# Kernel optimization log

Measured on AMD Instinct MI355X. Metric: run time of the kernel, lower is better.

The kernel has to match this reference:

```python
import jax, jax.numpy as jnp
import numpy as np

G = 7          # 7x7 feature map -> 49 nodes per image
N = G * G
K = 3          # knn_k
NEG_SLOPE = 0.2  # PyG GATConv default leaky_relu slope


def build_spatial_edges():
    # 8-neighborhood grid edges on the 7x7 map, directed (src -> dst)
    src, dst = [], []
    for r in range(G):
        for c in range(G):
            i = r * G + c
            for dr in (-1, 0, 1):
                for dc in (-1, 0, 1):
                    if dr == 0 and dc == 0:
                        continue
                    rr, cc = r + dr, c + dc
                    if 0 <= rr < G and 0 <= cc < G:
                        src.append(rr * G + cc)
                        dst.append(i)
    return np.array([src, dst], dtype=np.int32)

SPATIAL = build_spatial_edges()  # [2, 312]


def build_edges(x):
    """x: [B, N, F] node features -> (src, dst) each [B, E].
    Edges = spatial 8-neighborhood + feature-space kNN (k=3) + self-loops."""
    B = x.shape[0]
    sq = jnp.sum(x * x, axis=-1)                               # [B, N]
    d = sq[:, :, None] + sq[:, None, :] - 2.0 * jnp.einsum('bnf,bmf->bnm', x, x)
    d = d + jnp.eye(N, dtype=x.dtype) * 1e9                    # exclude self
    _, nbr = jax.lax.top_k(-d, K)                              # [B, N, K]
    knn_src = nbr.reshape(B, N * K)
    knn_dst = jnp.broadcast_to(jnp.repeat(jnp.arange(N, dtype=jnp.int32), K)[None], (B, N * K))
    sp = jnp.asarray(SPATIAL)
    Es = sp.shape[1]
    loops = jnp.arange(N, dtype=jnp.int32)
    src = jnp.concatenate([jnp.broadcast_to(sp[0][None], (B, Es)), knn_src.astype(jnp.int32),
                           jnp.broadcast_to(loops[None], (B, N))], axis=1)
    dst = jnp.concatenate([jnp.broadcast_to(sp[1][None], (B, Es)), knn_dst,
                           jnp.broadcast_to(loops[None], (B, N))], axis=1)
    return src, dst


def gat_layer(x, src, dst, W, a_src, a_dst, b, concat):
    """PyG-style GATConv (eval mode, no dropout). x: [N,F], src/dst: [E]."""
    H, C = a_src.shape
    h = (x @ W).reshape(N, H, C)                               # [N, H, C]
    es = jnp.sum(h * a_src[None], axis=-1)                     # [N, H]
    ed = jnp.sum(h * a_dst[None], axis=-1)                     # [N, H]
    e = jax.nn.leaky_relu(es[src] + ed[dst], NEG_SLOPE)        # [E, H]
    m = jax.ops.segment_max(e, dst, num_segments=N)            # [N, H]
    m = jnp.where(jnp.isfinite(m), m, 0.0)
    p = jnp.exp(e - m[dst])
    denom = jax.ops.segment_sum(p, dst, num_segments=N)
    alpha = p / jnp.maximum(denom[dst], 1e-16)                 # softmax over incoming edges
    out = jax.ops.segment_sum(alpha[:, :, None] * h[src], dst, num_segments=N)  # [N, H, C]
    out = out.reshape(N, H * C) if concat else out.mean(axis=1)
    return out + b


def setup_inputs() -> dict:
    key = jax.random.key(0)
    ks = jax.random.split(key, 14)
    B, F, Hd, Cd, O, NC = 256, 1024, 8, 128, 256, 14
    s = 0.05
    return {
        'feat_map': jax.random.normal(ks[0], (B, F, G, G), dtype=jnp.float32),
        'W1': jax.random.normal(ks[1], (F, Hd * Cd), dtype=jnp.float32) * s,
        'a_src1': jax.random.normal(ks[2], (Hd, Cd), dtype=jnp.float32) * s,
        'a_dst1': jax.random.normal(ks[3], (Hd, Cd), dtype=jnp.float32) * s,
        'b1': jnp.zeros((Hd * Cd,), dtype=jnp.float32),
        'W2': jax.random.normal(ks[4], (Hd * Cd, O), dtype=jnp.float32) * s,
        'a_src2': jax.random.normal(ks[5], (1, O), dtype=jnp.float32) * s,
        'a_dst2': jax.random.normal(ks[6], (1, O), dtype=jnp.float32) * s,
        'b2': jnp.zeros((O,), dtype=jnp.float32),
        'Wc1': jax.random.normal(ks[7], (O, O), dtype=jnp.float32) * s,
        'bc1': jnp.zeros((O,), dtype=jnp.float32),
        'Wc2': jax.random.normal(ks[8], (O, NC), dtype=jnp.float32) * s,
        'bc2': jnp.zeros((NC,), dtype=jnp.float32),
    }


def reference(feat_map, W1, a_src1, a_dst1, b1, W2, a_src2, a_dst2, b2, Wc1, bc1, Wc2, bc2):
    B = feat_map.shape[0]
    # backbone output relu + flatten 7x7 map into 49 nodes
    x = jax.nn.relu(feat_map).reshape(B, -1, N).transpose(0, 2, 1)  # [B, N, 1024]
    src, dst = build_edges(x)

    def per_graph(xg, sg, dg):
        h = jax.nn.elu(gat_layer(xg, sg, dg, W1, a_src1, a_dst1, b1, True))
        h = jax.nn.elu(gat_layer(h, sg, dg, W2, a_src2, a_dst2, b2, False))
        return h.mean(axis=0)                                   # global mean pool -> [256]

    pooled = jax.vmap(per_graph)(x, src, dst)                   # [B, 256]
    return jax.nn.relu(pooled @ Wc1 + bc1) @ Wc2 + bc2          # [B, 14]
```

## Files before the change

kernel.cpp:

```cpp
#include <hip/hip_runtime.h>

#define GDIM 7
#define NN 49
#define FDIM 1024
#define HD 8
#define CD 128
#define ODIM 256
#define NC 14
#define MAXE 12

typedef __attribute__((ext_vector_type(4))) float f32x4;
typedef __attribute__((ext_vector_type(8))) short s16x8;

struct us4 { unsigned short x, y, z, w; };

__device__ __forceinline__ unsigned short f2bf(float x) {
  unsigned u = __float_as_uint(x);
  return (unsigned short)((u + 0x7fffu + ((u >> 16) & 1u)) >> 16);
}
__device__ __forceinline__ float bf2f(unsigned short h) {
  return __uint_as_float((unsigned)h << 16);
}

#define GLOAD_LDS16(g, l)                                          \
  __builtin_amdgcn_global_load_lds(                                \
      (const __attribute__((address_space(1))) void*)(g),          \
      (__attribute__((address_space(3))) void*)(l), 16, 0, 0)

__global__ void __launch_bounds__(256) relu_transpose_kernel(
    const float* __restrict__ F, float* __restrict__ X,
    unsigned short* __restrict__ Xh, unsigned short* __restrict__ Xl) {
  const int b  = blockIdx.x >> 4;
  const int f0 = (blockIdx.x & 15) << 6;
  const int tid = threadIdx.x;
  __shared__ float lds[64 * NN];
  const float* src = F + (size_t)b * FDIM * NN + (size_t)f0 * NN;
  for (int idx = tid; idx < 64 * NN; idx += 256) lds[idx] = src[idx];
  __syncthreads();
  for (int pass = 0; pass < 13; pass++) {
    int n = pass * 4 + (tid >> 6);
    int fi = tid & 63;
    if (n < NN) {
      float v = lds[fi * NN + n];
      v = v > 0.f ? v : 0.f;
      size_t o = ((size_t)b * NN + n) * FDIM + f0 + fi;
      X[o] = v;
      unsigned short h = f2bf(v);
      Xh[o] = h;
      Xl[o] = f2bf(v - bf2f(h));
    }
  }
}

__global__ void __launch_bounds__(256) knn_kernel(
    const float* __restrict__ X, int* __restrict__ srcs_g,
    int* __restrict__ cnt_g) {
  const int b = blockIdx.x, tid = threadIdx.x;
  __shared__ float xs[56][68];
  __shared__ float gram[56][57];
  const float* Xb = X + (size_t)b * NN * FDIM;

  const int tr = tid / 14, tc = tid % 14;
  float acc[4][4];
#pragma unroll
  for (int i = 0; i < 4; i++)
#pragma unroll
    for (int j = 0; j < 4; j++) acc[i][j] = 0.f;

  for (int c0 = 0; c0 < FDIM; c0 += 64) {
    __syncthreads();
    for (int idx = tid; idx < NN * 16; idx += 256) {
      int n = idx >> 4, q = idx & 15;
      *(float4*)&xs[n][q << 2] =
          *(const float4*)&Xb[(size_t)n * FDIM + c0 + (q << 2)];
    }
    __syncthreads();
    if (tid < 196) {
#pragma unroll
      for (int k4 = 0; k4 < 64; k4 += 4) {
        float4 a[4], bb[4];
#pragma unroll
        for (int i = 0; i < 4; i++) a[i]  = *(const float4*)&xs[tr + 14 * i][k4];
#pragma unroll
        for (int j = 0; j < 4; j++) bb[j] = *(const float4*)&xs[tc + 14 * j][k4];
#pragma unroll
        for (int i = 0; i < 4; i++)
#pragma unroll
          for (int j = 0; j < 4; j++)
            acc[i][j] += a[i].x * bb[j].x + a[i].y * bb[j].y +
                         a[i].z * bb[j].z + a[i].w * bb[j].w;
      }
    }
  }
  if (tid < 196) {
#pragma unroll
    for (int i = 0; i < 4; i++)
#pragma unroll
      for (int j = 0; j < 4; j++) gram[tr + 14 * i][tc + 14 * j] = acc[i][j];
  }
  __syncthreads();
  if (tid < NN) {
    const int n = tid;
    const float sqn = gram[n][n];
    float d0 = 1e30f, d1 = 1e30f, d2 = 1e30f;
    int i0 = 0, i1 = 0, i2 = 0;
    for (int m = 0; m < NN; m++) {
      if (m == n) continue;
      float d = sqn + gram[m][m] - 2.f * gram[n][m];
      if (d < d0)      { d2=d1; i2=i1; d1=d0; i1=i0; d0=d; i0=m; }
      else if (d < d1) { d2=d1; i2=i1; d1=d;  i1=m; }
      else if (d < d2) { d2=d;  i2=m; }
    }
    int srcs[MAXE];
    int r = n / GDIM, c = n % GDIM, k = 0;
    for (int dr = -1; dr <= 1; dr++)
      for (int dc = -1; dc <= 1; dc++) {
        if (dr == 0 && dc == 0) continue;
        int rr = r + dr, cc = c + dc;
        if (rr >= 0 && rr < GDIM && cc >= 0 && cc < GDIM)
          srcs[k++] = rr * GDIM + cc;
      }
    srcs[k++] = i0; srcs[k++] = i1; srcs[k++] = i2;
    srcs[k++] = n;
    cnt_g[(size_t)b * NN + n] = k;
    for (int j = 0; j < MAXE; j++)
      srcs_g[((size_t)b * NN + n) * MAXE + j] = srcs[j < k ? j : 0];
  }
}

__global__ void __launch_bounds__(256) wconvT_kernel(
    const float* __restrict__ W, int K, int N,
    unsigned short* __restrict__ WhT, unsigned short* __restrict__ WlT) {
  __shared__ float t[64][65];
  const int nbx = N >> 6;
  const int bx = blockIdx.x % nbx, by = blockIdx.x / nbx;
  const int r0 = by << 6, c0 = bx << 6;
  const int tid = threadIdx.x;
#pragma unroll
  for (int i = 0; i < 16; i++) {
    int r = i * 4 + (tid >> 6), c = tid & 63;
    t[r][c] = W[(size_t)(r0 + r) * N + c0 + c];
  }
  __syncthreads();
#pragma unroll
  for (int i = 0; i < 16; i++) {
    int n = i * 4 + (tid >> 6);
    int k = tid & 63;
    float x = t[k][n];
    unsigned short h = f2bf(x);
    size_t o = (size_t)(c0 + n) * K + r0 + k;
    WhT[o] = h;
    WlT[o] = f2bf(x - bf2f(h));
  }
}

__global__ void __launch_bounds__(256) gemm_bf16x3(
    const unsigned short* __restrict__ A_h, const unsigned short* __restrict__ A_l,
    const unsigned short* __restrict__ BT_h, const unsigned short* __restrict__ BT_l,
    float* __restrict__ C, int M, int N, int K,
    const float* __restrict__ av, const float* __restrict__ dv,
    float* __restrict__ esp, float* __restrict__ edp) {
  __shared__ unsigned short sAh[128][64], sAl[128][64];
  __shared__ unsigned short sBh[128][64], sBl[128][64];
  const int tid = threadIdx.x;
  const int w = tid >> 6, lane = tid & 63;
  const int nbx = N >> 7;
  const int nwg = gridDim.x;
  const int q = nwg >> 3, r = nwg & 7;
  const int xcd = blockIdx.x & 7, loc = blockIdx.x >> 3;
  const int wg = (xcd < r) ? (xcd * (q + 1) + loc)
                           : (r * (q + 1) + (xcd - r) * q + loc);
  const int bx = wg % nbx, by = wg / nbx;
  const int row0 = by << 7, col0 = bx << 7;
  const int wr = (w >> 1) << 6, wc = (w & 1) << 6;
  const int sgr = lane >> 3;
  const int schunk = lane & 7;
  const int fr = lane & 15;
  const int fq = lane >> 4;

  f32x4 acc[4][4];
#pragma unroll
  for (int m = 0; m < 4; m++)
#pragma unroll
    for (int n = 0; n < 4; n++) acc[m][n] = (f32x4){0.f, 0.f, 0.f, 0.f};

  for (int k0 = 0; k0 < K; k0 += 64) {
    __syncthreads();
#pragma unroll
    for (int i = 0; i < 4; i++) {
      const int rbase = (w << 5) + (i << 3);
      const int gr = rbase + sgr;
      const int sc = schunk ^ (gr & 7);
      const size_t ga = (size_t)(row0 + gr) * K + k0 + (sc << 3);
      GLOAD_LDS16(A_h + ga, &sAh[rbase][0]);
      GLOAD_LDS16(A_l + ga, &sAl[rbase][0]);
      const size_t gb = (size_t)(col0 + gr) * K + k0 + (sc << 3);
      GLOAD_LDS16(BT_h + gb, &sBh[rbase][0]);
      GLOAD_LDS16(BT_l + gb, &sBl[rbase][0]);
    }
    __syncthreads();
#pragma unroll
    for (int ks = 0; ks < 2; ks++) {
      const int cb = (ks << 2) + fq;
      s16x8 ah[4], al[4], bh[4], bl[4];
#pragma unroll
      for (int m = 0; m < 4; m++) {
        const int ra = wr + (m << 4) + fr;
        const int ca = (cb ^ (ra & 7)) << 3;
        ah[m] = *(const s16x8*)&sAh[ra][ca];
        al[m] = *(const s16x8*)&sAl[ra][ca];
        const int rb = wc + (m << 4) + fr;
        const int cbn = (cb ^ (rb & 7)) << 3;
        bh[m] = *(const s16x8*)&sBh[rb][cbn];
        bl[m] = *(const s16x8*)&sBl[rb][cbn];
      }
#pragma unroll
      for (int m = 0; m < 4; m++)
#pragma unroll
        for (int n = 0; n < 4; n++) {
          acc[m][n] = __builtin_amdgcn_mfma_f32_16x16x32_bf16(ah[m], bh[n], acc[m][n], 0, 0, 0);
          acc[m][n] = __builtin_amdgcn_mfma_f32_16x16x32_bf16(ah[m], bl[n], acc[m][n], 0, 0, 0);
          acc[m][n] = __builtin_amdgcn_mfma_f32_16x16x32_bf16(al[m], bh[n], acc[m][n], 0, 0, 0);
        }
    }
  }
  const int crow = fq << 2, ccol = fr;
#pragma unroll
  for (int m = 0; m < 4; m++)
#pragma unroll
    for (int n = 0; n < 4; n++)
#pragma unroll
      for (int v = 0; v < 4; v++)
        C[(size_t)(row0 + wr + (m << 4) + crow + v) * N + col0 + wc + (n << 4) + ccol] =
            acc[m][n][v];

  const int pstride = N >> 6;
  const int part = (col0 + wc) >> 6;
  float asv[4], adv[4];
#pragma unroll
  for (int n = 0; n < 4; n++) {
    int cidx = col0 + wc + (n << 4) + fr;
    asv[n] = av[cidx];
    adv[n] = dv[cidx];
  }
#pragma unroll
  for (int m = 0; m < 4; m++)
#pragma unroll
    for (int v = 0; v < 4; v++) {
      float s = acc[m][0][v] * asv[0] + acc[m][1][v] * asv[1] +
                acc[m][2][v] * asv[2] + acc[m][3][v] * asv[3];
      float d = acc[m][0][v] * adv[0] + acc[m][1][v] * adv[1] +
                acc[m][2][v] * adv[2] + acc[m][3][v] * adv[3];
      s += __shfl_xor(s, 1); s += __shfl_xor(s, 2);
      s += __shfl_xor(s, 4); s += __shfl_xor(s, 8);
      d += __shfl_xor(d, 1); d += __shfl_xor(d, 2);
      d += __shfl_xor(d, 4); d += __shfl_xor(d, 8);
      if (fr == 0) {
        int row = row0 + wr + (m << 4) + (fq << 2) + v;
        esp[(size_t)row * pstride + part] = s;
        edp[(size_t)row * pstride + part] = d;
      }
    }
}

__global__ void __launch_bounds__(256) attn1_agg(
    const float* __restrict__ H, const int* __restrict__ srcs_g,
    const int* __restrict__ cnt_g, const float* __restrict__ es1p,
    const float* __restrict__ ed1p, const float* __restrict__ b1,
    unsigned short* __restrict__ Zh, unsigned short* __restrict__ Zl) {
  const int bid = blockIdx.x;
  const int b = bid / NN;
  const int tid = threadIdx.x;
  __shared__ int ss[MAXE];
  __shared__ float se[MAXE][HD];
  __shared__ float edv[HD];
  __shared__ float al[MAXE][HD];
  const int k = cnt_g[bid];
  if (tid < MAXE) ss[tid] = srcs_g[(size_t)bid * MAXE + tid];
  __syncthreads();
  if (tid < MAXE * HD) {
    int j = tid >> 3, h = tid & 7;
    size_t base = ((size_t)b * NN + ss[j]) * 16 + h * 2;
    se[j][h] = es1p[base] + es1p[base + 1];
  }
  if (tid >= 128 && tid < 128 + HD) {
    int h = tid - 128;
    size_t base = (size_t)bid * 16 + h * 2;
    edv[h] = ed1p[base] + ed1p[base + 1];
  }
  __syncthreads();
  if (tid < HD) {
    const int h = tid;
    float e[MAXE];
    float m = -1e30f;
#pragma unroll
    for (int j = 0; j < MAXE; j++) {
      if (j < k) {
        float v = se[j][h] + edv[h];
        v = v >= 0.f ? v : 0.2f * v;
        e[j] = v;
        m = fmaxf(m, v);
      }
    }
    float denom = 0.f;
#pragma unroll
    for (int j = 0; j < MAXE; j++) {
      if (j < k) { e[j] = expf(e[j] - m); denom += e[j]; }
    }
    float inv = 1.f / fmaxf(denom, 1e-16f);
#pragma unroll
    for (int j = 0; j < MAXE; j++) {
      if (j < k) al[j][h] = e[j] * inv;
    }
  }
  __syncthreads();
  const float4* Hb = (const float4*)(H + (size_t)b * NN * FDIM);
  const int h = tid >> 5;
  float4 acc = ((const float4*)b1)[tid];
  for (int j = 0; j < k; j++) {
    float a = al[j][h];
    float4 v = Hb[(size_t)ss[j] * (FDIM / 4) + tid];
    acc.x += a * v.x; acc.y += a * v.y; acc.z += a * v.z; acc.w += a * v.w;
  }
  acc.x = acc.x > 0.f ? acc.x : expm1f(acc.x);
  acc.y = acc.y > 0.f ? acc.y : expm1f(acc.y);
  acc.z = acc.z > 0.f ? acc.z : expm1f(acc.z);
  acc.w = acc.w > 0.f ? acc.w : expm1f(acc.w);
  us4 hv, lv;
  hv.x = f2bf(acc.x); lv.x = f2bf(acc.x - bf2f(hv.x));
  hv.y = f2bf(acc.y); lv.y = f2bf(acc.y - bf2f(hv.y));
  hv.z = f2bf(acc.z); lv.z = f2bf(acc.z - bf2f(hv.z));
  hv.w = f2bf(acc.w); lv.w = f2bf(acc.w - bf2f(hv.w));
  *(us4*)&Zh[(size_t)bid * FDIM + (tid << 2)] = hv;
  *(us4*)&Zl[(size_t)bid * FDIM + (tid << 2)] = lv;
}

__global__ void __launch_bounds__(256) attn2_agg(
    const float* __restrict__ H2, const int* __restrict__ srcs_g,
    const int* __restrict__ cnt_g, const float* __restrict__ es2p,
    const float* __restrict__ ed2p, const float* __restrict__ b2,
    float* __restrict__ Z2) {
  const int bid = blockIdx.x;
  const int b = bid / NN;
  const int tid = threadIdx.x;
  __shared__ int ss[MAXE];
  __shared__ float se[MAXE];
  __shared__ float al[MAXE];
  const int k = cnt_g[bid];
  if (tid < MAXE) ss[tid] = srcs_g[(size_t)bid * MAXE + tid];
  __syncthreads();
  if (tid < MAXE) {
    size_t base = ((size_t)b * NN + ss[tid]) * 4;
    se[tid] = es2p[base] + es2p[base + 1] + es2p[base + 2] + es2p[base + 3];
  }
  __syncthreads();
  if (tid == 0) {
    size_t base = (size_t)bid * 4;
    float ed = ed2p[base] + ed2p[base + 1] + ed2p[base + 2] + ed2p[base + 3];
    float e[MAXE];
    float m = -1e30f;
#pragma unroll
    for (int j = 0; j < MAXE; j++) {
      if (j < k) {
        float v = se[j] + ed;
        v = v >= 0.f ? v : 0.2f * v;
        e[j] = v;
        m = fmaxf(m, v);
      }
    }
    float denom = 0.f;
#pragma unroll
    for (int j = 0; j < MAXE; j++) {
      if (j < k) { e[j] = expf(e[j] - m); denom += e[j]; }
    }
    float inv = 1.f / fmaxf(denom, 1e-16f);
#pragma unroll
    for (int j = 0; j < MAXE; j++) {
      if (j < k) al[j] = e[j] * inv;
    }
  }
  __syncthreads();
  const float* Hb = H2 + (size_t)b * NN * ODIM;
  float acc = b2[tid];
  for (int j = 0; j < k; j++)
    acc += al[j] * Hb[(size_t)ss[j] * ODIM + tid];
  acc = acc > 0.f ? acc : expm1f(acc);
  Z2[(size_t)bid * ODIM + tid] = acc;
}

__global__ void __launch_bounds__(256) classifier_kernel(
    const float* __restrict__ Z2, const float* __restrict__ Wc1,
    const float* __restrict__ bc1, const float* __restrict__ Wc2,
    const float* __restrict__ bc2, float* __restrict__ out) {
  const int b = blockIdx.x, tid = threadIdx.x;
  __shared__ float p[ODIM];
  __shared__ float t[ODIM];
  float s = 0.f;
  for (int i = 0; i < NN; i++)
    s += Z2[((size_t)b * NN + i) * ODIM + tid];
  p[tid] = s * (1.f / 49.f);
  __syncthreads();
  float a = bc1[tid];
  for (int c = 0; c < ODIM; c++) a += p[c] * Wc1[(size_t)c * ODIM + tid];
  t[tid] = a > 0.f ? a : 0.f;
  __syncthreads();
  if (tid < NC) {
    float o = bc2[tid];
    for (int j = 0; j < ODIM; j++) o += t[j] * Wc2[(size_t)j * NC + tid];
    out[(size_t)b * NC + tid] = o;
  }
}

extern "C" void kernel_launch(void* const* d_in, const int* in_sizes, int n_in,
                              void* d_out, int out_size, void* d_ws, size_t ws_size,
                              hipStream_t stream) {
  const float* feat   = (const float*)d_in[0];
  const float* W1     = (const float*)d_in[1];
  const float* a_src1 = (const float*)d_in[2];
  const float* a_dst1 = (const float*)d_in[3];
  const float* b1     = (const float*)d_in[4];
  const float* W2     = (const float*)d_in[5];
  const float* a_src2 = (const float*)d_in[6];
  const float* a_dst2 = (const float*)d_in[7];
  const float* b2     = (const float*)d_in[8];
  const float* Wc1    = (const float*)d_in[9];
  const float* bc1    = (const float*)d_in[10];
  const float* Wc2    = (const float*)d_in[11];
  const float* bc2    = (const float*)d_in[12];

  const int B = in_sizes[0] / (FDIM * NN);
  const int M = B * NN;

  const size_t xE = (size_t)M * FDIM;
  float* X  = (float*)d_ws;
  float* H1 = X + xE;
  unsigned short* Xh = (unsigned short*)(H1 + xE);
  unsigned short* Xl = Xh + xE;
  unsigned short* W1hT = Xl + xE;
  unsigned short* W1lT = W1hT + (size_t)FDIM * FDIM;
  unsigned short* W2hT = W1lT + (size_t)FDIM * FDIM;
  unsigned short* W2lT = W2hT + (size_t)ODIM * FDIM;
  int*   srcs_g = (int*)(W2lT + (size_t)ODIM * FDIM);
  int*   cnt_g  = srcs_g + (size_t)M * MAXE;
  float* es1p   = (float*)(cnt_g + M);
  float* ed1p   = es1p + (size_t)M * 16;
  float* es2p   = ed1p + (size_t)M * 16;
  float* ed2p   = es2p + (size_t)M * 4;
  float* H2  = X;
  float* Z2  = H1;
  unsigned short* Z1h = Xh;
  unsigned short* Z1l = Xl;

  relu_transpose_kernel<<<B * 16, 256, 0, stream>>>(feat, X, Xh, Xl);
  knn_kernel<<<B, 256, 0, stream>>>(X, srcs_g, cnt_g);
  wconvT_kernel<<<(FDIM / 64) * (FDIM / 64), 256, 0, stream>>>(W1, FDIM, FDIM, W1hT, W1lT);
  wconvT_kernel<<<(FDIM / 64) * (ODIM / 64), 256, 0, stream>>>(W2, FDIM, ODIM, W2hT, W2lT);
  gemm_bf16x3<<<(M / 128) * (FDIM / 128), 256, 0, stream>>>(
      Xh, Xl, W1hT, W1lT, H1, M, FDIM, FDIM, a_src1, a_dst1, es1p, ed1p);
  attn1_agg<<<M, 256, 0, stream>>>(H1, srcs_g, cnt_g, es1p, ed1p, b1, Z1h, Z1l);
  gemm_bf16x3<<<(M / 128) * (ODIM / 128), 256, 0, stream>>>(
      Z1h, Z1l, W2hT, W2lT, H2, M, ODIM, FDIM, a_src2, a_dst2, es2p, ed2p);
  attn2_agg<<<M, 256, 0, stream>>>(H2, srcs_g, cnt_g, es2p, ed2p, b2, Z2);
  classifier_kernel<<<B, 256, 0, stream>>>(Z2, Wc1, bc1, Wc2, bc2, (float*)d_out);
}
```

Baseline: 314.9 us.

## Merge prep kernels and co-schedule kNN with first GEMM in one launch

Relu-transpose and both weight conversions are combined into one pre-kernel launch, and the fp32 X buffer is no longer written. The kNN now reads raw features directly, applying relu and a transpose in shared memory. It runs as extra workgroups inside the first GEMM launch so the two overlap. This cuts launch count and a large fp32 write/read, at the cost of a 64KB LDS allocation for the kNN blocks and hardcoded block counts in pre_kernel.

```diff
diff --git a/kernel.cpp b/kernel.cpp
--- a/kernel.cpp
+++ b/kernel.cpp
@@ -11,6 +11,7 @@
 
 typedef __attribute__((ext_vector_type(4))) float f32x4;
 typedef __attribute__((ext_vector_type(8))) short s16x8;
+typedef unsigned short ushort_t;
 
 struct us4 { unsigned short x, y, z, w; };
 
@@ -27,13 +28,14 @@
       (const __attribute__((address_space(1))) void*)(g),          \
       (__attribute__((address_space(3))) void*)(l), 16, 0, 0)
 
-__global__ void __launch_bounds__(256) relu_transpose_kernel(
-    const float* __restrict__ F, float* __restrict__ X,
-    unsigned short* __restrict__ Xh, unsigned short* __restrict__ Xl) {
-  const int b  = blockIdx.x >> 4;
-  const int f0 = (blockIdx.x & 15) << 6;
+
+__device__ void relu_body(char* smem, int blk, const float* __restrict__ F,
+                          unsigned short* __restrict__ Xh,
+                          unsigned short* __restrict__ Xl) {
+  float* lds = (float*)smem;
+  const int b  = blk >> 4;
+  const int f0 = (blk & 15) << 6;
   const int tid = threadIdx.x;
-  __shared__ float lds[64 * NN];
   const float* src = F + (size_t)b * FDIM * NN + (size_t)f0 * NN;
   for (int idx = tid; idx < 64 * NN; idx += 256) lds[idx] = src[idx];
   __syncthreads();
@@ -44,7 +46,6 @@
       float v = lds[fi * NN + n];
       v = v > 0.f ? v : 0.f;
       size_t o = ((size_t)b * NN + n) * FDIM + f0 + fi;
-      X[o] = v;
       unsigned short h = f2bf(v);
       Xh[o] = h;
       Xl[o] = f2bf(v - bf2f(h));
@@ -52,14 +53,38 @@
   }
 }
 
-__global__ void __launch_bounds__(256) knn_kernel(
-    const float* __restrict__ X, int* __restrict__ srcs_g,
-    int* __restrict__ cnt_g) {
-  const int b = blockIdx.x, tid = threadIdx.x;
-  __shared__ float xs[56][68];
-  __shared__ float gram[56][57];
-  const float* Xb = X + (size_t)b * NN * FDIM;
-
+__device__ void wconvT_body(const float* __restrict__ W, int K, int N,
+                            unsigned short* __restrict__ WhT,
+                            unsigned short* __restrict__ WlT, int blk,
+                            float* t ) {
+  const int nbx = N >> 6;
+  const int bx = blk % nbx, by = blk / nbx;
+  const int r0 = by << 6, c0 = bx << 6;
+  const int tid = threadIdx.x;
+#pragma unroll
+  for (int i = 0; i < 16; i++) {
+    int r = i * 4 + (tid >> 6), c = tid & 63;
+    t[r * 65 + c] = W[(size_t)(r0 + r) * N + c0 + c];
+  }
+  __syncthreads();
+#pragma unroll
+  for (int i = 0; i < 16; i++) {
+    int n = i * 4 + (tid >> 6);
+    int k = tid & 63;
+    float x = t[k * 65 + n];
+    unsigned short h = f2bf(x);
+    size_t o = (size_t)(c0 + n) * K + r0 + k;
+    WhT[o] = h;
+    WlT[o] = f2bf(x - bf2f(h));
+  }
+}
+
+__device__ void knn_body(char* smem, int b, const float* __restrict__ F,
+                         int* __restrict__ srcs_g, int* __restrict__ cnt_g) {
+  float* raw = (float*)smem;
+  float (*xs)[68] = (float(*)[68])(smem + 12544);
+  float (*gram)[57] = (float(*)[57])(smem + 27776);
+  const int tid = threadIdx.x;
   const int tr = tid / 14, tc = tid % 14;
   float acc[4][4];
 #pragma unroll
@@ -68,11 +93,16 @@
     for (int j = 0; j < 4; j++) acc[i][j] = 0.f;
 
   for (int c0 = 0; c0 < FDIM; c0 += 64) {
+    const float* src = F + ((size_t)b * FDIM + c0) * NN;
     __syncthreads();
-    for (int idx = tid; idx < NN * 16; idx += 256) {
-      int n = idx >> 4, q = idx & 15;
-      *(float4*)&xs[n][q << 2] =
-          *(const float4*)&Xb[(size_t)n * FDIM + c0 + (q << 2)];
+    for (int idx = tid; idx < 64 * NN; idx += 256) {
+      float v = src[idx];
+      raw[idx] = v > 0.f ? v : 0.f;
+    }
+    __syncthreads();
+    for (int idx = tid; idx < 64 * NN; idx += 256) {
+      int cc = idx & 63, n = idx >> 6;
+      xs[n][cc] = raw[cc * NN + n];
     }
     __syncthreads();
     if (tid < 196) {
@@ -128,46 +158,22 @@
   }
 }
 
-__global__ void __launch_bounds__(256) wconvT_kernel(
-    const float* __restrict__ W, int K, int N,
-    unsigned short* __restrict__ WhT, unsigned short* __restrict__ WlT) {
-  __shared__ float t[64][65];
-  const int nbx = N >> 6;
-  const int bx = blockIdx.x % nbx, by = blockIdx.x / nbx;
-  const int r0 = by << 6, c0 = bx << 6;
-  const int tid = threadIdx.x;
-#pragma unroll
-  for (int i = 0; i < 16; i++) {
-    int r = i * 4 + (tid >> 6), c = tid & 63;
-    t[r][c] = W[(size_t)(r0 + r) * N + c0 + c];
-  }
-  __syncthreads();
-#pragma unroll
-  for (int i = 0; i < 16; i++) {
-    int n = i * 4 + (tid >> 6);
-    int k = tid & 63;
-    float x = t[k][n];
-    unsigned short h = f2bf(x);
-    size_t o = (size_t)(c0 + n) * K + r0 + k;
-    WhT[o] = h;
-    WlT[o] = f2bf(x - bf2f(h));
-  }
-}
-
-__global__ void __launch_bounds__(256) gemm_bf16x3(
+__device__ void gemm_body(
+    char* smem, int bid, int NWG,
     const unsigned short* __restrict__ A_h, const unsigned short* __restrict__ A_l,
     const unsigned short* __restrict__ BT_h, const unsigned short* __restrict__ BT_l,
     float* __restrict__ C, int M, int N, int K,
     const float* __restrict__ av, const float* __restrict__ dv,
     float* __restrict__ esp, float* __restrict__ edp) {
-  __shared__ unsigned short sAh[128][64], sAl[128][64];
-  __shared__ unsigned short sBh[128][64], sBl[128][64];
+  unsigned short (*sAh)[64] = (unsigned short(*)[64])(smem);
+  unsigned short (*sAl)[64] = (unsigned short(*)[64])(smem + 16384);
+  unsigned short (*sBh)[64] = (unsigned short(*)[64])(smem + 32768);
+  unsigned short (*sBl)[64] = (unsigned short(*)[64])(smem + 49152);
   const int tid = threadIdx.x;
   const int w = tid >> 6, lane = tid & 63;
   const int nbx = N >> 7;
-  const int nwg = gridDim.x;
-  const int q = nwg >> 3, r = nwg & 7;
-  const int xcd = blockIdx.x & 7, loc = blockIdx.x >> 3;
+  const int q = NWG >> 3, r = NWG & 7;
+  const int xcd = bid & 7, loc = bid >> 3;
   const int wg = (xcd < r) ? (xcd * (q + 1) + loc)
                            : (r * (q + 1) + (xcd - r) * q + loc);
   const int bx = wg % nbx, by = wg / nbx;
@@ -261,6 +267,51 @@
         edp[(size_t)row * pstride + part] = d;
       }
     }
+}
+
+
+__global__ void __launch_bounds__(256) pre_kernel(
+    const float* __restrict__ F, unsigned short* __restrict__ Xh,
+    unsigned short* __restrict__ Xl, const float* __restrict__ W1,
+    unsigned short* __restrict__ W1hT, unsigned short* __restrict__ W1lT,
+    const float* __restrict__ W2, unsigned short* __restrict__ W2hT,
+    unsigned short* __restrict__ W2lT) {
+  __shared__ __align__(16) char smem[16640];
+  if (blockIdx.x < 4096) {
+    relu_body(smem, blockIdx.x, F, Xh, Xl);
+  } else if (blockIdx.x < 4352) {
+    wconvT_body(W1, FDIM, FDIM, W1hT, W1lT, blockIdx.x - 4096, (float*)smem);
+  } else {
+    wconvT_body(W2, FDIM, ODIM, W2hT, W2lT, blockIdx.x - 4352, (float*)smem);
+  }
+}
+
+__global__ void __launch_bounds__(256) gemm1_knn_kernel(
+    const unsigned short* __restrict__ A_h, const unsigned short* __restrict__ A_l,
+    const unsigned short* __restrict__ BT_h, const unsigned short* __restrict__ BT_l,
+    float* __restrict__ C, int M, int N, int K, int NWG,
+    const float* __restrict__ av, const float* __restrict__ dv,
+    float* __restrict__ esp, float* __restrict__ edp,
+    const float* __restrict__ F, int* __restrict__ srcs_g,
+    int* __restrict__ cnt_g) {
+  __shared__ __align__(16) char smem[65536];
+  if ((int)blockIdx.x < NWG) {
+    gemm_body(smem, blockIdx.x, NWG, A_h, A_l, BT_h, BT_l, C, M, N, K,
+              av, dv, esp, edp);
+  } else {
+    knn_body(smem, blockIdx.x - NWG, F, srcs_g, cnt_g);
+  }
+}
+
+__global__ void __launch_bounds__(256) gemm_kernel(
+    const unsigned short* __restrict__ A_h, const unsigned short* __restrict__ A_l,
+    const unsigned short* __restrict__ BT_h, const unsigned short* __restrict__ BT_l,
+    float* __restrict__ C, int M, int N, int K,
+    const float* __restrict__ av, const float* __restrict__ dv,
+    float* __restrict__ esp, float* __restrict__ edp) {
+  __shared__ __align__(16) char smem[65536];
+  gemm_body(smem, blockIdx.x, gridDim.x, A_h, A_l, BT_h, BT_l, C, M, N, K,
+            av, dv, esp, edp);
 }
 
 __global__ void __launch_bounds__(256) attn1_agg(
@@ -432,8 +483,7 @@
   const int M = B * NN;
 
   const size_t xE = (size_t)M * FDIM;
-  float* X  = (float*)d_ws;
-  float* H1 = X + xE;
+  float* H1 = (float*)d_ws;
   unsigned short* Xh = (unsigned short*)(H1 + xE);
   unsigned short* Xl = Xh + xE;
   unsigned short* W1hT = Xl + xE;
@@ -446,19 +496,21 @@
   float* ed1p   = es1p + (size_t)M * 16;
   float* es2p   = ed1p + (size_t)M * 16;
   float* ed2p   = es2p + (size_t)M * 4;
-  float* H2  = X;
-  float* Z2  = H1;
+  float* H2  = H1;
+  float* Z2  = H1 + (size_t)M * ODIM;
   unsigned short* Z1h = Xh;
   unsigned short* Z1l = Xl;
 
-  relu_transpose_kernel<<<B * 16, 256, 0, stream>>>(feat, X, Xh, Xl);
-  knn_kernel<<<B, 256, 0, stream>>>(X, srcs_g, cnt_g);
-  wconvT_kernel<<<(FDIM / 64) * (FDIM / 64), 256, 0, stream>>>(W1, FDIM, FDIM, W1hT, W1lT);
-  wconvT_kernel<<<(FDIM / 64) * (ODIM / 64), 256, 0, stream>>>(W2, FDIM, ODIM, W2hT, W2lT);
-  gemm_bf16x3<<<(M / 128) * (FDIM / 128), 256, 0, stream>>>(
-      Xh, Xl, W1hT, W1lT, H1, M, FDIM, FDIM, a_src1, a_dst1, es1p, ed1p);
+  const int NWG1 = (M / 128) * (FDIM / 128);
+  const int NWG2 = (M / 128) * (ODIM / 128);
+
+  pre_kernel<<<4416, 256, 0, stream>>>(feat, Xh, Xl, W1, W1hT, W1lT,
+                                       W2, W2hT, W2lT);
+  gemm1_knn_kernel<<<NWG1 + B, 256, 0, stream>>>(
+      Xh, Xl, W1hT, W1lT, H1, M, FDIM, FDIM, NWG1,
+      a_src1, a_dst1, es1p, ed1p, feat, srcs_g, cnt_g);
   attn1_agg<<<M, 256, 0, stream>>>(H1, srcs_g, cnt_g, es1p, ed1p, b1, Z1h, Z1l);
-  gemm_bf16x3<<<(M / 128) * (ODIM / 128), 256, 0, stream>>>(
+  gemm_kernel<<<NWG2, 256, 0, stream>>>(
       Z1h, Z1l, W2hT, W2lT, H2, M, ODIM, FDIM, a_src2, a_dst2, es2p, ed2p);
   attn2_agg<<<M, 256, 0, stream>>>(H2, srcs_g, cnt_g, es2p, ed2p, b2, Z2);
   classifier_kernel<<<B, 256, 0, stream>>>(Z2, Wc1, bc1, Wc2, bc2, (float*)d_out);
```

Result: slower. 432.2 us (+37.2%).
